# Optimization experiments

Measured on AMD Instinct MI355X. Metric: run time of the kernel, lower is better.

Reference implementation:

```python
import jax, jax.numpy as jnp
import numpy as np


@jax.custom_vjp
def spike(u):
    # Surrogate_BP_Function.forward: u.ge(0).float()
    return (u >= 0).astype(u.dtype)

def _spike_fwd(u):
    return spike(u), u

def _spike_bwd(u, g):
    # backward: g * 0.3 * relu(1 - |u|) * 2
    return (g * 0.6 * jnp.maximum(1.0 - jnp.abs(u), 0.0),)

spike.defvjp(_spike_fwd, _spike_bwd)


def setup_inputs() -> dict:
    key = jax.random.key(0)
    ks = jax.random.split(key, 5)
    B, T, I, H = 64, 512, 256, 512
    x = jax.random.normal(ks[0], (B, T, I), jnp.float32)
    conv1_w = jax.random.normal(ks[1], (H, I, 3), jnp.float32) * 0.1
    conv1_b = jax.random.normal(ks[2], (H,), jnp.float32) * 0.1
    conv2_w = jax.random.normal(ks[3], (H, H, 3), jnp.float32) * 0.1
    conv2_b = jax.random.normal(ks[4], (H,), jnp.float32) * 0.1
    th1 = jnp.ones((), jnp.float32)
    th2 = jnp.ones((), jnp.float32)
    return {"x": x, "conv1_w": conv1_w, "conv1_b": conv1_b,
            "conv2_w": conv2_w, "conv2_b": conv2_b, "th1": th1, "th2": th2}


def reference(x, conv1_w, conv1_b, conv2_w, conv2_b, th1, th2):
    leak = 1.0  # leak_mem from __init__
    # Conv1d(k=3, pad=1) on a length-1 sequence uses only the center tap.
    W1 = conv1_w[:, :, 1]  # [H, I]
    W2 = conv2_w[:, :, 1]  # [H, H]
    B, T, _ = x.shape
    H = W1.shape[0]
    # Precompute input drive for layer 1 (depends only on x[t]).
    z1 = jnp.einsum('bti,hi->bth', x, W1) + conv1_b  # [B, T, H]

    def step(carry, z1_t):
        m1, m2 = carry
        m1 = leak * m1 + z1_t
        thr1 = m1 / th1 - 1.0
        s1 = spike(thr1)
        m1 = m1 - th1 * (thr1 > 0).astype(x.dtype)
        m2 = leak * m2 + s1 @ W2.T + conv2_b
        thr2 = m2 / th2 - 1.0
        s2 = spike(thr2)
        m2 = m2 - th2 * (thr2 > 0).astype(x.dtype)
        return (m1, m2), s2

    init = (jnp.zeros((B, H), x.dtype), jnp.zeros((B, H), x.dtype))
    _, out_t = jax.lax.scan(step, init, jnp.swapaxes(z1, 0, 1))  # [T, B, H]
    return jnp.swapaxes(out_t, 0, 1)  # [B, T, H]
```

## Files before the change

### kernel.cpp

```cpp
#include <hip/hip_runtime.h>

#define BATCH 64
#define TSTEPS 512
#define IDIM 256
#define HDIM 512
#define MROWS (BATCH * TSTEPS)

typedef __attribute__((address_space(1))) const void gvoid;
typedef __attribute__((address_space(3))) void lvoid;

__device__ __forceinline__ void gl2lds16(const void* g, void* l) {
    __builtin_amdgcn_global_load_lds((gvoid*)g, (lvoid*)l, 16, 0, 0);
}

__global__ void extract_weights(const float* __restrict__ c1w,
                                const float* __restrict__ c2w,
                                float* __restrict__ W1T,
                                float* __restrict__ W2T) {
    int tid = blockIdx.x * 256 + threadIdx.x;
    if (tid < IDIM * HDIM) {
        int i = tid >> 9;
        int h = tid & 511;
        W1T[tid] = c1w[(h * IDIM + i) * 3 + 1];
    }
    if (tid < HDIM * HDIM) {
        int h = tid >> 9;
        int j = tid & 511;
        W2T[tid] = c2w[(j * HDIM + h) * 3 + 1];
    }
}

#define BM 256
#define BN 128
#define BK 16

__global__ __launch_bounds__(256, 2) void gemm_f32(const float* __restrict__ A,
                                                   const float* __restrict__ BT,
                                                   const float* __restrict__ bias,
                                                   float* __restrict__ C,
                                                   int K, int addBias) {
    __shared__ __align__(16) float As[BK * BM];
    __shared__ __align__(16) float Bs[BK * BN];

    const int N = HDIM;
    int tid  = threadIdx.x;
    int row0 = blockIdx.x * BM;
    int col0 = blockIdx.y * BN;
    int hg = tid >> 4;
    int gg = tid & 15;

    float acc[16][8];
#pragma unroll
    for (int i = 0; i < 16; i++)
#pragma unroll
        for (int j = 0; j < 8; j++) acc[i][j] = 0.0f;

    const float* ap = A + (size_t)(row0 + tid) * K;

    const char* bp = (const char*)(BT + (size_t)(tid >> 5) * N + col0) + (tid & 31) * 16;
    char* bld = (char*)Bs + tid * 16;
    const size_t bRow8 = (size_t)8 * N * sizeof(float);

    for (int k0 = 0; k0 < K; k0 += BK) {
        gl2lds16(bp,         bld);
        gl2lds16(bp + bRow8, bld + 4096);
        float4 a0 = *(const float4*)(ap);
        float4 a1 = *(const float4*)(ap + 4);
        float4 a2 = *(const float4*)(ap + 8);
        float4 a3 = *(const float4*)(ap + 12);
        ap += BK;
        bp += (size_t)BK * N * sizeof(float);
        As[ 0 * BM + tid] = a0.x;  As[ 1 * BM + tid] = a0.y;
        As[ 2 * BM + tid] = a0.z;  As[ 3 * BM + tid] = a0.w;
        As[ 4 * BM + tid] = a1.x;  As[ 5 * BM + tid] = a1.y;
        As[ 6 * BM + tid] = a1.z;  As[ 7 * BM + tid] = a1.w;
        As[ 8 * BM + tid] = a2.x;  As[ 9 * BM + tid] = a2.y;
        As[10 * BM + tid] = a2.z;  As[11 * BM + tid] = a2.w;
        As[12 * BM + tid] = a3.x;  As[13 * BM + tid] = a3.y;
        As[14 * BM + tid] = a3.z;  As[15 * BM + tid] = a3.w;
        __syncthreads();

#pragma unroll
        for (int k = 0; k < BK; k++) {
            float4 av[4];
#pragma unroll
            for (int s = 0; s < 4; s++)
                av[s] = *(const float4*)&As[k * BM + hg * 4 + s * 64];
            float4 bv[2];
#pragma unroll
            for (int t = 0; t < 2; t++)
                bv[t] = *(const float4*)&Bs[k * BN + gg * 4 + t * 64];
            const float* a16 = (const float*)av;
            const float* b8  = (const float*)bv;
#pragma unroll
            for (int i = 0; i < 16; i++)
#pragma unroll
                for (int j = 0; j < 8; j++)
                    acc[i][j] = fmaf(a16[i], b8[j], acc[i][j]);
        }
        __syncthreads();
    }

    float bb[8];
#pragma unroll
    for (int t = 0; t < 2; t++)
#pragma unroll
        for (int j = 0; j < 4; j++)
            bb[t * 4 + j] = addBias ? bias[col0 + gg * 4 + t * 64 + j] : 0.0f;
#pragma unroll
    for (int s = 0; s < 4; s++)
#pragma unroll
        for (int i = 0; i < 4; i++) {
            int row = row0 + hg * 4 + s * 64 + i;
            float* cp = &C[(size_t)row * N + col0 + gg * 4];
#pragma unroll
            for (int t = 0; t < 2; t++) {
                float4 v;
                v.x = acc[s * 4 + i][t * 4 + 0] + bb[t * 4 + 0];
                v.y = acc[s * 4 + i][t * 4 + 1] + bb[t * 4 + 1];
                v.z = acc[s * 4 + i][t * 4 + 2] + bb[t * 4 + 2];
                v.w = acc[s * 4 + i][t * 4 + 3] + bb[t * 4 + 3];
                *(float4*)(cp + t * 64) = v;
            }
        }
}

__global__ void lif_scan1(const float* __restrict__ z1,
                          float* __restrict__ s1,
                          const float* __restrict__ th_p) {
    int gtid = blockIdx.x * blockDim.x + threadIdx.x;
    int b = gtid >> 9;
    int h = gtid & 511;
    float th = *th_p;
    const float* zp = z1 + (size_t)b * TSTEPS * HDIM + h;
    float* sp = s1 + (size_t)b * TSTEPS * HDIM + h;
    float m = 0.0f;
    float bufA[16], bufB[16];
#pragma unroll
    for (int i = 0; i < 16; i++) bufA[i] = zp[(size_t)i * HDIM];
    for (int t0 = 0; t0 < TSTEPS; t0 += 32) {
#pragma unroll
        for (int i = 0; i < 16; i++) bufB[i] = zp[(size_t)(t0 + 16 + i) * HDIM];
        {
            float ss[16];
#pragma unroll
            for (int i = 0; i < 16; i++) {
                m += bufA[i];
                float thr = m / th - 1.0f;
                ss[i] = (thr >= 0.0f) ? 1.0f : 0.0f;
                if (thr > 0.0f) m -= th;
            }
#pragma unroll
            for (int i = 0; i < 16; i++) sp[(size_t)(t0 + i) * HDIM] = ss[i];
        }
        if (t0 + 32 < TSTEPS) {
#pragma unroll
            for (int i = 0; i < 16; i++) bufA[i] = zp[(size_t)(t0 + 32 + i) * HDIM];
        }
        {
            float ss[16];
#pragma unroll
            for (int i = 0; i < 16; i++) {
                m += bufB[i];
                float thr = m / th - 1.0f;
                ss[i] = (thr >= 0.0f) ? 1.0f : 0.0f;
                if (thr > 0.0f) m -= th;
            }
#pragma unroll
            for (int i = 0; i < 16; i++) sp[(size_t)(t0 + 16 + i) * HDIM] = ss[i];
        }
    }
}

__global__ void lif_scan2(const float* __restrict__ raw,
                          const float* __restrict__ b2,
                          const float* __restrict__ th_p,
                          float* __restrict__ out) {
    int gtid = blockIdx.x * blockDim.x + threadIdx.x;
    int b = gtid >> 9;
    int j = gtid & 511;
    float th = *th_p;
    float bias = b2[j];
    const float* rp = raw + (size_t)b * TSTEPS * HDIM + j;
    float* op = out + (size_t)b * TSTEPS * HDIM + j;
    float m = 0.0f;
    float bufA[16], bufB[16];
#pragma unroll
    for (int i = 0; i < 16; i++) bufA[i] = rp[(size_t)i * HDIM];
    for (int t0 = 0; t0 < TSTEPS; t0 += 32) {
#pragma unroll
        for (int i = 0; i < 16; i++) bufB[i] = rp[(size_t)(t0 + 16 + i) * HDIM];
        {
            float ss[16];
#pragma unroll
            for (int i = 0; i < 16; i++) {
                m = (m + bufA[i]) + bias;
                float thr = m / th - 1.0f;
                ss[i] = (thr >= 0.0f) ? 1.0f : 0.0f;
                if (thr > 0.0f) m -= th;
            }
#pragma unroll
            for (int i = 0; i < 16; i++) op[(size_t)(t0 + i) * HDIM] = ss[i];
        }
        if (t0 + 32 < TSTEPS) {
#pragma unroll
            for (int i = 0; i < 16; i++) bufA[i] = rp[(size_t)(t0 + 32 + i) * HDIM];
        }
        {
            float ss[16];
#pragma unroll
            for (int i = 0; i < 16; i++) {
                m = (m + bufB[i]) + bias;
                float thr = m / th - 1.0f;
                ss[i] = (thr >= 0.0f) ? 1.0f : 0.0f;
                if (thr > 0.0f) m -= th;
            }
#pragma unroll
            for (int i = 0; i < 16; i++) op[(size_t)(t0 + 16 + i) * HDIM] = ss[i];
        }
    }
}

extern "C" void kernel_launch(void* const* d_in, const int* in_sizes, int n_in,
                              void* d_out, int out_size, void* d_ws, size_t ws_size,
                              hipStream_t stream) {
    const float* x    = (const float*)d_in[0];
    const float* c1w  = (const float*)d_in[1];
    const float* c1b  = (const float*)d_in[2];
    const float* c2w  = (const float*)d_in[3];
    const float* c2b  = (const float*)d_in[4];
    const float* th1  = (const float*)d_in[5];
    const float* th2  = (const float*)d_in[6];
    float* out = (float*)d_out;

    float* W1T  = (float*)d_ws;
    float* W2T  = W1T + IDIM * HDIM;
    float* bufA = W2T + HDIM * HDIM;
    float* bufS = bufA + (size_t)MROWS * HDIM;

    extract_weights<<<(HDIM * HDIM + 255) / 256, 256, 0, stream>>>(c1w, c2w, W1T, W2T);

    {
        dim3 grid(MROWS / BM, HDIM / BN);
        gemm_f32<<<grid, 256, 0, stream>>>(x, W1T, c1b, bufA, IDIM, 1);
    }

    lif_scan1<<<MROWS / 64, 64, 0, stream>>>(bufA, bufS, th1);

    {
        dim3 grid(MROWS / BM, HDIM / BN);
        gemm_f32<<<grid, 256, 0, stream>>>(bufS, W2T, (const float*)nullptr, bufA, HDIM, 0);
    }

    lif_scan2<<<MROWS / 64, 64, 0, stream>>>(bufA, c2b, th2, out);
}
```

Baseline: 432.9 us.

## Split GEMM into retiled layer-1 kernel and transposed-spike layer-2 kernel

Replaces the shared GEMM with two specialised kernels. The first GEMM uses 128x128 tiles with an 8x8 per-thread micro-tile arranged per wave. The second GEMM takes a transposed spike matrix that lif_scan1 now writes as float4 rows along time. It uses single-wave blocks that read A rows directly from global memory into registers and stage only B in LDS. The intent is better occupancy and less LDS traffic for the spike GEMM, but the direct scalar global loads of A may be poorly coalesced and the second GEMM has low arithmetic intensity per block.

```diff
diff --git a/kernel.cpp b/kernel.cpp
--- a/kernel.cpp
+++ b/kernel.cpp
@@ -30,110 +30,183 @@
     }
 }
 
-#define BM 256
-#define BN 128
-#define BK 16
-
-__global__ __launch_bounds__(256, 2) void gemm_f32(const float* __restrict__ A,
-                                                   const float* __restrict__ BT,
-                                                   const float* __restrict__ bias,
-                                                   float* __restrict__ C,
-                                                   int K, int addBias) {
-    __shared__ __align__(16) float As[BK * BM];
-    __shared__ __align__(16) float Bs[BK * BN];
+#define BM1 128
+#define BN1 128
+#define BK1 16
+
+__global__ __launch_bounds__(256, 2) void gemm_g1(const float* __restrict__ A,
+                                                  const float* __restrict__ BT,
+                                                  const float* __restrict__ bias,
+                                                  float* __restrict__ C,
+                                                  int K) {
+    __shared__ __align__(16) float As[BK1 * BM1];
+    __shared__ __align__(16) float Bs[BK1 * BN1];
 
     const int N = HDIM;
     int tid  = threadIdx.x;
-    int row0 = blockIdx.x * BM;
-    int col0 = blockIdx.y * BN;
-    int hg = tid >> 4;
-    int gg = tid & 15;
-
-    float acc[16][8];
-#pragma unroll
-    for (int i = 0; i < 16; i++)
+    int lane = tid & 63;
+    int wave = tid >> 6;
+    int row0 = blockIdx.x * BM1;
+    int col0 = blockIdx.y * BN1;
+    int wm = (wave >> 1) * 64;
+    int wn = (wave & 1) * 64;
+    int mbase = wm + (lane >> 3) * 8;
+    int nbase = wn + (lane & 7) * 8;
+
+    float acc[8][8];
+#pragma unroll
+    for (int i = 0; i < 8; i++)
 #pragma unroll
         for (int j = 0; j < 8; j++) acc[i][j] = 0.0f;
 
-    const float* ap = A + (size_t)(row0 + tid) * K;
+    int ar = tid >> 1;
+    int ak = (tid & 1) * 8;
+    const float* ap = A + (size_t)(row0 + ar) * K + ak;
 
     const char* bp = (const char*)(BT + (size_t)(tid >> 5) * N + col0) + (tid & 31) * 16;
     char* bld = (char*)Bs + tid * 16;
     const size_t bRow8 = (size_t)8 * N * sizeof(float);
 
-    for (int k0 = 0; k0 < K; k0 += BK) {
-        gl2lds16(bp,         bld);
+    for (int k0 = 0; k0 < K; k0 += BK1) {
+        gl2lds16(bp, bld);
         gl2lds16(bp + bRow8, bld + 4096);
         float4 a0 = *(const float4*)(ap);
         float4 a1 = *(const float4*)(ap + 4);
-        float4 a2 = *(const float4*)(ap + 8);
-        float4 a3 = *(const float4*)(ap + 12);
-        ap += BK;
-        bp += (size_t)BK * N * sizeof(float);
-        As[ 0 * BM + tid] = a0.x;  As[ 1 * BM + tid] = a0.y;
-        As[ 2 * BM + tid] = a0.z;  As[ 3 * BM + tid] = a0.w;
-        As[ 4 * BM + tid] = a1.x;  As[ 5 * BM + tid] = a1.y;
-        As[ 6 * BM + tid] = a1.z;  As[ 7 * BM + tid] = a1.w;
-        As[ 8 * BM + tid] = a2.x;  As[ 9 * BM + tid] = a2.y;
-        As[10 * BM + tid] = a2.z;  As[11 * BM + tid] = a2.w;
-        As[12 * BM + tid] = a3.x;  As[13 * BM + tid] = a3.y;
-        As[14 * BM + tid] = a3.z;  As[15 * BM + tid] = a3.w;
+        ap += BK1;
+        bp += (size_t)BK1 * N * sizeof(float);
+        As[(ak + 0) * BM1 + ar] = a0.x;
+        As[(ak + 1) * BM1 + ar] = a0.y;
+        As[(ak + 2) * BM1 + ar] = a0.z;
+        As[(ak + 3) * BM1 + ar] = a0.w;
+        As[(ak + 4) * BM1 + ar] = a1.x;
+        As[(ak + 5) * BM1 + ar] = a1.y;
+        As[(ak + 6) * BM1 + ar] = a1.z;
+        As[(ak + 7) * BM1 + ar] = a1.w;
         __syncthreads();
 
 #pragma unroll
-        for (int k = 0; k < BK; k++) {
-            float4 av[4];
-#pragma unroll
-            for (int s = 0; s < 4; s++)
-                av[s] = *(const float4*)&As[k * BM + hg * 4 + s * 64];
-            float4 bv[2];
-#pragma unroll
-            for (int t = 0; t < 2; t++)
-                bv[t] = *(const float4*)&Bs[k * BN + gg * 4 + t * 64];
-            const float* a16 = (const float*)av;
-            const float* b8  = (const float*)bv;
-#pragma unroll
-            for (int i = 0; i < 16; i++)
+        for (int k = 0; k < BK1; k++) {
+            float4 av0 = *(const float4*)&As[k * BM1 + mbase];
+            float4 av1 = *(const float4*)&As[k * BM1 + mbase + 4];
+            float4 bv0 = *(const float4*)&Bs[k * BN1 + nbase];
+            float4 bv1 = *(const float4*)&Bs[k * BN1 + nbase + 4];
+            float a8[8] = {av0.x, av0.y, av0.z, av0.w, av1.x, av1.y, av1.z, av1.w};
+            float b8[8] = {bv0.x, bv0.y, bv0.z, bv0.w, bv1.x, bv1.y, bv1.z, bv1.w};
+#pragma unroll
+            for (int i = 0; i < 8; i++)
 #pragma unroll
                 for (int j = 0; j < 8; j++)
-                    acc[i][j] = fmaf(a16[i], b8[j], acc[i][j]);
+                    acc[i][j] = fmaf(a8[i], b8[j], acc[i][j]);
         }
         __syncthreads();
     }
 
     float bb[8];
 #pragma unroll
-    for (int t = 0; t < 2; t++)
-#pragma unroll
-        for (int j = 0; j < 4; j++)
-            bb[t * 4 + j] = addBias ? bias[col0 + gg * 4 + t * 64 + j] : 0.0f;
-#pragma unroll
-    for (int s = 0; s < 4; s++)
-#pragma unroll
-        for (int i = 0; i < 4; i++) {
-            int row = row0 + hg * 4 + s * 64 + i;
-            float* cp = &C[(size_t)row * N + col0 + gg * 4];
-#pragma unroll
-            for (int t = 0; t < 2; t++) {
-                float4 v;
-                v.x = acc[s * 4 + i][t * 4 + 0] + bb[t * 4 + 0];
-                v.y = acc[s * 4 + i][t * 4 + 1] + bb[t * 4 + 1];
-                v.z = acc[s * 4 + i][t * 4 + 2] + bb[t * 4 + 2];
-                v.w = acc[s * 4 + i][t * 4 + 3] + bb[t * 4 + 3];
-                *(float4*)(cp + t * 64) = v;
-            }
-        }
+    for (int j = 0; j < 8; j++) bb[j] = bias[col0 + nbase + j];
+#pragma unroll
+    for (int i = 0; i < 8; i++) {
+        int row = row0 + mbase + i;
+        float4* cp = (float4*)&C[(size_t)row * N + col0 + nbase];
+        cp[0] = (float4){acc[i][0] + bb[0], acc[i][1] + bb[1],
+                         acc[i][2] + bb[2], acc[i][3] + bb[3]};
+        cp[1] = (float4){acc[i][4] + bb[4], acc[i][5] + bb[5],
+                         acc[i][6] + bb[6], acc[i][7] + bb[7]};
+    }
+}
+
+#define G2_BN 256
+#define G2_BK 8
+
+__global__ __launch_bounds__(64, 4) void gemm_g2(const float* __restrict__ AT,
+                                                 const float* __restrict__ BT,
+                                                 float* __restrict__ C) {
+    __shared__ __align__(16) float Bs[G2_BK * G2_BN];
+
+    const int N = HDIM;
+    const int K = HDIM;
+    int lane  = threadIdx.x;
+    int row0  = blockIdx.x * 16;
+    int col0  = blockIdx.y * G2_BN;
+    int lane4 = lane * 4;
+
+    float acc[16][4];
+#pragma unroll
+    for (int i = 0; i < 16; i++)
+#pragma unroll
+        for (int j = 0; j < 4; j++) acc[i][j] = 0.0f;
+
+    float a0[16], a1[16];
+    {
+        const float* p = AT + row0;
+#pragma unroll
+        for (int i = 0; i < 16; i++) a0[i] = p[i];
+    }
+
+    const char* bsrc0 = (const char*)(BT + col0) + lane * 16;
+    char* bld = (char*)Bs + lane * 16;
+
+    for (int k0 = 0; k0 < K; k0 += G2_BK) {
+#pragma unroll
+        for (int q = 0; q < G2_BK; q++)
+            gl2lds16(bsrc0 + (size_t)(k0 + q) * N * sizeof(float),
+                     bld + q * 1024);
+        __syncthreads();
+
+#pragma unroll
+        for (int k = 0; k < G2_BK; k += 2) {
+            int kk = k0 + k;
+            {
+                const float* p = AT + (size_t)(kk + 1) * MROWS + row0;
+#pragma unroll
+                for (int i = 0; i < 16; i++) a1[i] = p[i];
+            }
+            {
+                float4 bv = *(const float4*)&Bs[k * G2_BN + lane4];
+#pragma unroll
+                for (int i = 0; i < 16; i++) {
+                    acc[i][0] = fmaf(a0[i], bv.x, acc[i][0]);
+                    acc[i][1] = fmaf(a0[i], bv.y, acc[i][1]);
+                    acc[i][2] = fmaf(a0[i], bv.z, acc[i][2]);
+                    acc[i][3] = fmaf(a0[i], bv.w, acc[i][3]);
+                }
+            }
+            {
+                int kn = kk + 2; if (kn > K - 1) kn = K - 1;
+                const float* p = AT + (size_t)kn * MROWS + row0;
+#pragma unroll
+                for (int i = 0; i < 16; i++) a0[i] = p[i];
+            }
+            {
+                float4 bv = *(const float4*)&Bs[(k + 1) * G2_BN + lane4];
+#pragma unroll
+                for (int i = 0; i < 16; i++) {
+                    acc[i][0] = fmaf(a1[i], bv.x, acc[i][0]);
+                    acc[i][1] = fmaf(a1[i], bv.y, acc[i][1]);
+                    acc[i][2] = fmaf(a1[i], bv.z, acc[i][2]);
+                    acc[i][3] = fmaf(a1[i], bv.w, acc[i][3]);
+                }
+            }
+        }
+        __syncthreads();
+    }
+
+#pragma unroll
+    for (int i = 0; i < 16; i++) {
+        *(float4*)&C[(size_t)(row0 + i) * N + col0 + lane4] =
+            (float4){acc[i][0], acc[i][1], acc[i][2], acc[i][3]};
+    }
 }
 
 __global__ void lif_scan1(const float* __restrict__ z1,
-                          float* __restrict__ s1,
+                          float* __restrict__ s1T,
                           const float* __restrict__ th_p) {
     int gtid = blockIdx.x * blockDim.x + threadIdx.x;
     int b = gtid >> 9;
     int h = gtid & 511;
     float th = *th_p;
     const float* zp = z1 + (size_t)b * TSTEPS * HDIM + h;
-    float* sp = s1 + (size_t)b * TSTEPS * HDIM + h;
+    float* sp = s1T + (size_t)h * MROWS + (size_t)b * TSTEPS;
     float m = 0.0f;
     float bufA[16], bufB[16];
 #pragma unroll
@@ -151,7 +224,9 @@
                 if (thr > 0.0f) m -= th;
             }
 #pragma unroll
-            for (int i = 0; i < 16; i++) sp[(size_t)(t0 + i) * HDIM] = ss[i];
+            for (int v = 0; v < 4; v++)
+                *(float4*)&sp[t0 + v * 4] =
+                    (float4){ss[v * 4], ss[v * 4 + 1], ss[v * 4 + 2], ss[v * 4 + 3]};
         }
         if (t0 + 32 < TSTEPS) {
 #pragma unroll
@@ -167,7 +242,9 @@
                 if (thr > 0.0f) m -= th;
             }
 #pragma unroll
-            for (int i = 0; i < 16; i++) sp[(size_t)(t0 + 16 + i) * HDIM] = ss[i];
+            for (int v = 0; v < 4; v++)
+                *(float4*)&sp[t0 + 16 + v * 4] =
+                    (float4){ss[v * 4], ss[v * 4 + 1], ss[v * 4 + 2], ss[v * 4 + 3]};
         }
     }
 }
@@ -241,15 +318,15 @@
     extract_weights<<<(HDIM * HDIM + 255) / 256, 256, 0, stream>>>(c1w, c2w, W1T, W2T);
 
     {
-        dim3 grid(MROWS / BM, HDIM / BN);
-        gemm_f32<<<grid, 256, 0, stream>>>(x, W1T, c1b, bufA, IDIM, 1);
+        dim3 grid(MROWS / BM1, HDIM / BN1);
+        gemm_g1<<<grid, 256, 0, stream>>>(x, W1T, c1b, bufA, IDIM);
     }
 
     lif_scan1<<<MROWS / 64, 64, 0, stream>>>(bufA, bufS, th1);
 
     {
-        dim3 grid(MROWS / BM, HDIM / BN);
-        gemm_f32<<<grid, 256, 0, stream>>>(bufS, W2T, (const float*)nullptr, bufA, HDIM, 0);
+        dim3 grid(MROWS / 16, HDIM / G2_BN);
+        gemm_g2<<<grid, 64, 0, stream>>>(bufS, W2T, bufA);
     }
 
     lif_scan2<<<MROWS / 64, 64, 0, stream>>>(bufA, c2b, th2, out);
```

After: 435.7 us. Within noise of the previous version (+0.7%).

## Double-buffer FP32 GEMM shared tiles and remap to 128x128 wave-tiled blocks

Applied to the files above, without the earlier changes.

The GEMM tile shrinks from 256x128 to 128x128, with each wave owning a 64x64 sub-tile and each lane computing an 8x8 block. Shared memory for A and B is double-buffered so the next K-slice is loaded from global memory while the current slice is computed, leaving one barrier per iteration. The aim is to hide global-load latency and launch more blocks. The trade-off is lower arithmetic intensity per thread, since there are 64 accumulators instead of 128, and twice the LDS footprint.

```diff
diff --git a/kernel.cpp b/kernel.cpp
--- a/kernel.cpp
+++ b/kernel.cpp
@@ -30,99 +30,123 @@
     }
 }
 
-#define BM 256
-#define BN 128
-#define BK 16
+#define BM1 128
+#define BN1 128
+#define BK1 16
 
 __global__ __launch_bounds__(256, 2) void gemm_f32(const float* __restrict__ A,
                                                    const float* __restrict__ BT,
                                                    const float* __restrict__ bias,
                                                    float* __restrict__ C,
                                                    int K, int addBias) {
-    __shared__ __align__(16) float As[BK * BM];
-    __shared__ __align__(16) float Bs[BK * BN];
+    __shared__ __align__(16) float As[2][BK1 * BM1];
+    __shared__ __align__(16) float Bs[2][BK1 * BN1];
 
     const int N = HDIM;
     int tid  = threadIdx.x;
-    int row0 = blockIdx.x * BM;
-    int col0 = blockIdx.y * BN;
-    int hg = tid >> 4;
-    int gg = tid & 15;
-
-    float acc[16][8];
-#pragma unroll
-    for (int i = 0; i < 16; i++)
+    int lane = tid & 63;
+    int wave = tid >> 6;
+    int row0 = blockIdx.x * BM1;
+    int col0 = blockIdx.y * BN1;
+    int wm = (wave >> 1) * 64;
+    int wn = (wave & 1) * 64;
+    int mbase = wm + (lane >> 3) * 8;
+    int nbase = wn + (lane & 7) * 8;
+
+    float acc[8][8];
+#pragma unroll
+    for (int i = 0; i < 8; i++)
 #pragma unroll
         for (int j = 0; j < 8; j++) acc[i][j] = 0.0f;
 
-    const float* ap = A + (size_t)(row0 + tid) * K;
+    int ar = tid >> 1;
+    int ak = (tid & 1) * 8;
+    const float* ap = A + (size_t)(row0 + ar) * K + ak;
 
     const char* bp = (const char*)(BT + (size_t)(tid >> 5) * N + col0) + (tid & 31) * 16;
-    char* bld = (char*)Bs + tid * 16;
     const size_t bRow8 = (size_t)8 * N * sizeof(float);
-
-    for (int k0 = 0; k0 < K; k0 += BK) {
-        gl2lds16(bp,         bld);
+    int ldsOff = tid * 16;
+
+    {
+        char* bld = (char*)&Bs[0][0] + ldsOff;
+        gl2lds16(bp, bld);
         gl2lds16(bp + bRow8, bld + 4096);
+        bp += (size_t)BK1 * N * sizeof(float);
         float4 a0 = *(const float4*)(ap);
         float4 a1 = *(const float4*)(ap + 4);
-        float4 a2 = *(const float4*)(ap + 8);
-        float4 a3 = *(const float4*)(ap + 12);
-        ap += BK;
-        bp += (size_t)BK * N * sizeof(float);
-        As[ 0 * BM + tid] = a0.x;  As[ 1 * BM + tid] = a0.y;
-        As[ 2 * BM + tid] = a0.z;  As[ 3 * BM + tid] = a0.w;
-        As[ 4 * BM + tid] = a1.x;  As[ 5 * BM + tid] = a1.y;
-        As[ 6 * BM + tid] = a1.z;  As[ 7 * BM + tid] = a1.w;
-        As[ 8 * BM + tid] = a2.x;  As[ 9 * BM + tid] = a2.y;
-        As[10 * BM + tid] = a2.z;  As[11 * BM + tid] = a2.w;
-        As[12 * BM + tid] = a3.x;  As[13 * BM + tid] = a3.y;
-        As[14 * BM + tid] = a3.z;  As[15 * BM + tid] = a3.w;
+        ap += BK1;
+        float* asb = &As[0][0];
+        asb[(ak + 0) * BM1 + ar] = a0.x;
+        asb[(ak + 1) * BM1 + ar] = a0.y;
+        asb[(ak + 2) * BM1 + ar] = a0.z;
+        asb[(ak + 3) * BM1 + ar] = a0.w;
+        asb[(ak + 4) * BM1 + ar] = a1.x;
+        asb[(ak + 5) * BM1 + ar] = a1.y;
+        asb[(ak + 6) * BM1 + ar] = a1.z;
+        asb[(ak + 7) * BM1 + ar] = a1.w;
+    }
+    __syncthreads();
+
+    const int nIter = K / BK1;
+    for (int it = 0; it < nIter; it++) {
+        int cur = it & 1;
+        int nxt = cur ^ 1;
+        const bool has = (it + 1 < nIter);
+        float4 na0, na1;
+        if (has) {
+            char* bld = (char*)&Bs[nxt][0] + ldsOff;
+            gl2lds16(bp, bld);
+            gl2lds16(bp + bRow8, bld + 4096);
+            bp += (size_t)BK1 * N * sizeof(float);
+            na0 = *(const float4*)(ap);
+            na1 = *(const float4*)(ap + 4);
+            ap += BK1;
+        }
+
+        const float* asb = &As[cur][0];
+        const float* bsb = &Bs[cur][0];
+#pragma unroll
+        for (int k = 0; k < BK1; k++) {
+            float4 av0 = *(const float4*)&asb[k * BM1 + mbase];
+            float4 av1 = *(const float4*)&asb[k * BM1 + mbase + 4];
+            float4 bv0 = *(const float4*)&bsb[k * BN1 + nbase];
+            float4 bv1 = *(const float4*)&bsb[k * BN1 + nbase + 4];
+            float a8[8] = {av0.x, av0.y, av0.z, av0.w, av1.x, av1.y, av1.z, av1.w};
+            float b8[8] = {bv0.x, bv0.y, bv0.z, bv0.w, bv1.x, bv1.y, bv1.z, bv1.w};
+#pragma unroll
+            for (int i = 0; i < 8; i++)
+#pragma unroll
+                for (int j = 0; j < 8; j++)
+                    acc[i][j] = fmaf(a8[i], b8[j], acc[i][j]);
+        }
+
+        if (has) {
+            float* asn = &As[nxt][0];
+            asn[(ak + 0) * BM1 + ar] = na0.x;
+            asn[(ak + 1) * BM1 + ar] = na0.y;
+            asn[(ak + 2) * BM1 + ar] = na0.z;
+            asn[(ak + 3) * BM1 + ar] = na0.w;
+            asn[(ak + 4) * BM1 + ar] = na1.x;
+            asn[(ak + 5) * BM1 + ar] = na1.y;
+            asn[(ak + 6) * BM1 + ar] = na1.z;
+            asn[(ak + 7) * BM1 + ar] = na1.w;
+        }
         __syncthreads();
-
-#pragma unroll
-        for (int k = 0; k < BK; k++) {
-            float4 av[4];
-#pragma unroll
-            for (int s = 0; s < 4; s++)
-                av[s] = *(const float4*)&As[k * BM + hg * 4 + s * 64];
-            float4 bv[2];
-#pragma unroll
-            for (int t = 0; t < 2; t++)
-                bv[t] = *(const float4*)&Bs[k * BN + gg * 4 + t * 64];
-            const float* a16 = (const float*)av;
-            const float* b8  = (const float*)bv;
-#pragma unroll
-            for (int i = 0; i < 16; i++)
-#pragma unroll
-                for (int j = 0; j < 8; j++)
-                    acc[i][j] = fmaf(a16[i], b8[j], acc[i][j]);
-        }
-        __syncthreads();
     }
 
     float bb[8];
 #pragma unroll
-    for (int t = 0; t < 2; t++)
-#pragma unroll
-        for (int j = 0; j < 4; j++)
-            bb[t * 4 + j] = addBias ? bias[col0 + gg * 4 + t * 64 + j] : 0.0f;
-#pragma unroll
-    for (int s = 0; s < 4; s++)
-#pragma unroll
-        for (int i = 0; i < 4; i++) {
-            int row = row0 + hg * 4 + s * 64 + i;
-            float* cp = &C[(size_t)row * N + col0 + gg * 4];
-#pragma unroll
-            for (int t = 0; t < 2; t++) {
-                float4 v;
-                v.x = acc[s * 4 + i][t * 4 + 0] + bb[t * 4 + 0];
-                v.y = acc[s * 4 + i][t * 4 + 1] + bb[t * 4 + 1];
-                v.z = acc[s * 4 + i][t * 4 + 2] + bb[t * 4 + 2];
-                v.w = acc[s * 4 + i][t * 4 + 3] + bb[t * 4 + 3];
-                *(float4*)(cp + t * 64) = v;
-            }
-        }
+    for (int j = 0; j < 8; j++)
+        bb[j] = addBias ? bias[col0 + nbase + j] : 0.0f;
+#pragma unroll
+    for (int i = 0; i < 8; i++) {
+        int row = row0 + mbase + i;
+        float4* cp = (float4*)&C[(size_t)row * N + col0 + nbase];
+        cp[0] = (float4){acc[i][0] + bb[0], acc[i][1] + bb[1],
+                         acc[i][2] + bb[2], acc[i][3] + bb[3]};
+        cp[1] = (float4){acc[i][4] + bb[4], acc[i][5] + bb[5],
+                         acc[i][6] + bb[6], acc[i][7] + bb[7]};
+    }
 }
 
 __global__ void lif_scan1(const float* __restrict__ z1,
@@ -241,14 +265,14 @@
     extract_weights<<<(HDIM * HDIM + 255) / 256, 256, 0, stream>>>(c1w, c2w, W1T, W2T);
 
     {
-        dim3 grid(MROWS / BM, HDIM / BN);
+        dim3 grid(MROWS / BM1, HDIM / BN1);
         gemm_f32<<<grid, 256, 0, stream>>>(x, W1T, c1b, bufA, IDIM, 1);
     }
 
     lif_scan1<<<MROWS / 64, 64, 0, stream>>>(bufA, bufS, th1);
 
     {
-        dim3 grid(MROWS / BM, HDIM / BN);
+        dim3 grid(MROWS / BM1, HDIM / BN1);
         gemm_f32<<<grid, 256, 0, stream>>>(bufS, W2T, (const float*)nullptr, bufA, HDIM, 0);
     }
 
```

Result: slower. 1.640 ms (+278.8%).
